# Optimization experiments

Measured on AMD Instinct MI355X. Metric: run time of the kernel, lower is better.

The kernel has to match this reference:

```python
import jax, jax.numpy as jnp
import numpy as np

D_MODEL = 1024
D_STATE = 32
EXPAND = 2
D_INNER = D_MODEL * EXPAND          # 2048
DT_RANK = D_MODEL // 16             # 64
LN_EPS = 1e-5


def setup_inputs() -> dict:
    key = jax.random.key(0)
    ks = jax.random.split(key, 9)
    s = 0.02
    x = jax.random.normal(ks[0], (2, 2048, D_MODEL), dtype=jnp.float32)
    W_in = jax.random.normal(ks[1], (2 * D_INNER, D_MODEL), dtype=jnp.float32) * s
    W_x = jax.random.normal(ks[2], (DT_RANK + 2 * D_STATE, D_INNER), dtype=jnp.float32) * s
    W_dt = jax.random.normal(ks[3], (D_INNER, DT_RANK), dtype=jnp.float32) * s
    b_dt = jax.random.normal(ks[4], (D_INNER,), dtype=jnp.float32) * s
    A_real0 = jax.random.normal(ks[5], (D_INNER, D_STATE), dtype=jnp.float32) * 0.5
    A_log_real = jnp.log(jnp.clip(-A_real0, 1e-4, None))
    A_imag = jax.random.normal(ks[6], (D_INNER, D_STATE), dtype=jnp.float32) * 0.1
    D_param = jnp.ones((D_INNER,), dtype=jnp.float32)
    W_out = jax.random.normal(ks[7], (D_MODEL, D_INNER), dtype=jnp.float32) * s
    ln_g = jnp.ones((D_MODEL,), dtype=jnp.float32)
    ln_b = jnp.zeros((D_MODEL,), dtype=jnp.float32)
    return {"x": x, "W_in": W_in, "W_x": W_x, "W_dt": W_dt, "b_dt": b_dt,
            "A_log_real": A_log_real, "A_imag": A_imag, "D_param": D_param,
            "W_out": W_out, "ln_g": ln_g, "ln_b": ln_b}


def _forward(x, W_in, W_x, W_dt, b_dt, A_log_real, A_imag, D_param, W_out, ln_g, ln_b):
    B, T, _ = x.shape
    residual = x
    # LayerNorm
    mu = jnp.mean(x, axis=-1, keepdims=True)
    var = jnp.mean((x - mu) ** 2, axis=-1, keepdims=True)
    xn = (x - mu) * jax.lax.rsqrt(var + LN_EPS) * ln_g + ln_b
    # in_proj -> (x_ssm, z)
    xz = jnp.einsum('btd,ed->bte', xn, W_in)            # (B,T,2*d_inner)
    x_ssm, z = jnp.split(xz, 2, axis=-1)
    # x_proj -> dt_low, B, C
    x_dbl = jnp.einsum('bte,re->btr', x_ssm, W_x)        # (B,T,dt_rank+2*d_state)
    dt_low = x_dbl[..., :DT_RANK]
    B_param = x_dbl[..., DT_RANK:DT_RANK + D_STATE]      # (B,T,N)
    C_param = x_dbl[..., DT_RANK + D_STATE:]             # (B,T,N)
    dt = jax.nn.softplus(jnp.einsum('btr,er->bte', dt_low, W_dt) + b_dt)  # (B,T,d_inner)
    # A = -exp(A_log_real) + i * A_imag, complex state split into (hr, hi)
    Ar = -jnp.exp(A_log_real)                             # (d_inner,N)
    Ai = A_imag

    def step(carry, inp):
        hr, hi = carry                                    # (B,d_inner,N)
        dt_t, B_t, C_t, x_t = inp                         # (B,d_inner),(B,N),(B,N),(B,d_inner)
        dtE = dt_t[:, :, None]                            # (B,d_inner,1)
        scale = jnp.exp(Ar[None] * dtE)
        ang = Ai[None] * dtE
        dAr = scale * jnp.cos(ang)
        dAi = scale * jnp.sin(ang)
        dBx = (dt_t * x_t)[:, :, None] * B_t[:, None, :]  # real input injection
        hr2 = dAr * hr - dAi * hi + dBx
        hi2 = dAr * hi + dAi * hr
        y = jnp.sum(hr2 * C_t[:, None, :], axis=-1)       # real part of (h * C).sum
        return (hr2, hi2), y

    h0 = jnp.zeros((B, D_INNER, D_STATE), dtype=x.dtype)
    xs = (jnp.transpose(dt, (1, 0, 2)), jnp.transpose(B_param, (1, 0, 2)),
          jnp.transpose(C_param, (1, 0, 2)), jnp.transpose(x_ssm, (1, 0, 2)))
    _, ys = jax.lax.scan(step, (h0, h0), xs)              # (T,B,d_inner)
    y = jnp.transpose(ys, (1, 0, 2)) + D_param * x_ssm
    y = y * jax.nn.silu(z)
    out = jnp.einsum('bte,de->btd', y, W_out)
    return residual + out  # dropout is identity at eval


def reference(x, W_in, W_x, W_dt, b_dt, A_log_real, A_imag, D_param, W_out, ln_g, ln_b):
    return _forward(x, W_in, W_x, W_dt, b_dt, A_log_real, A_imag, D_param, W_out, ln_g, ln_b)
```

## Files before the change

kernel.cpp:

```cpp
#include <hip/hip_runtime.h>
#include <math.h>

#define D_MODEL 1024
#define D_STATE 32
#define D_INNER 2048
#define DT_RANK 64
#define BT 4096
#define LN_EPS 1e-5f

typedef __attribute__((ext_vector_type(8))) short short8;
typedef __attribute__((ext_vector_type(4))) float f32x4;
typedef const __attribute__((address_space(1))) void* gp_t;
typedef __attribute__((address_space(3))) void* lp_t;

__device__ __forceinline__ ushort bf16r(float f) {
    unsigned u = __float_as_uint(f);
    u += 0x7fff + ((u >> 16) & 1);
    return (ushort)(u >> 16);
}

__global__ __launch_bounds__(256) void cvt_bf16(const float* __restrict__ in,
                                                ushort* __restrict__ out, int n4) {
    int i = blockIdx.x * 256 + threadIdx.x;
    if (i >= n4) return;
    float4 v = ((const float4*)in)[i];
    ushort4 o;
    o.x = bf16r(v.x); o.y = bf16r(v.y); o.z = bf16r(v.z); o.w = bf16r(v.w);
    ((ushort4*)out)[i] = o;
}

__global__ __launch_bounds__(256) void ln_kernel(const float* __restrict__ x,
                                                 const float* __restrict__ g,
                                                 const float* __restrict__ b,
                                                 ushort* __restrict__ xn) {
    int row = blockIdx.x;
    const float4* xr = (const float4*)(x + (size_t)row * D_MODEL);
    float4 v = xr[threadIdx.x];
    float s  = v.x + v.y + v.z + v.w;
    float ss = v.x*v.x + v.y*v.y + v.z*v.z + v.w*v.w;
    #pragma unroll
    for (int off = 32; off > 0; off >>= 1) {
        s  += __shfl_down(s,  off, 64);
        ss += __shfl_down(ss, off, 64);
    }
    __shared__ float rs[4], rss[4];
    int wave = threadIdx.x >> 6;
    if ((threadIdx.x & 63) == 0) { rs[wave] = s; rss[wave] = ss; }
    __syncthreads();
    s  = rs[0] + rs[1] + rs[2] + rs[3];
    ss = rss[0] + rss[1] + rss[2] + rss[3];
    float mu  = s * (1.f / D_MODEL);
    float var = ss * (1.f / D_MODEL) - mu * mu;
    float inv = rsqrtf(var + LN_EPS);
    float4 gv = ((const float4*)g)[threadIdx.x];
    float4 bv = ((const float4*)b)[threadIdx.x];
    ushort4 o;
    o.x = bf16r((v.x - mu) * inv * gv.x + bv.x);
    o.y = bf16r((v.y - mu) * inv * gv.y + bv.y);
    o.z = bf16r((v.z - mu) * inv * gv.z + bv.z);
    o.w = bf16r((v.w - mu) * inv * gv.w + bv.w);
    ((ushort4*)(xn + (size_t)row * D_MODEL))[threadIdx.x] = o;
}

template<int RESID>
__global__ __launch_bounds__(256) void gemm_bt_bf16(
    const ushort* __restrict__ A, const ushort* __restrict__ B,
    float* __restrict__ C, int ldc, int K,
    const float* __restrict__ resid)
{
    __shared__ __align__(16) ushort As[128 * 32];
    __shared__ __align__(16) ushort Bs[128 * 32];
    int tid = threadIdx.x;
    int bm = blockIdx.x * 128, bn = blockIdx.y * 128;
    int wave = tid >> 6, lane = tid & 63;
    int wm = (wave & 1) * 64, wn = (wave >> 1) * 64;
    int quad = lane >> 4, m16 = lane & 15;
    int grow = tid >> 2;
    int gcol = (tid & 3) * 8;
    const size_t a0 = (size_t)(bm + grow) * K + gcol;
    const size_t b0 = (size_t)(bn + grow) * K + gcol;
    char* asw = (char*)As + wave * 1024;
    char* bsw = (char*)Bs + wave * 1024;

    f32x4 acc[4][4] = {};
    for (int k0 = 0; k0 < K; k0 += 32) {
        __builtin_amdgcn_global_load_lds((gp_t)(A + a0 + k0),                 (lp_t)asw,          16, 0, 0);
        __builtin_amdgcn_global_load_lds((gp_t)(A + a0 + (size_t)64*K + k0),  (lp_t)(asw + 4096), 16, 0, 0);
        __builtin_amdgcn_global_load_lds((gp_t)(B + b0 + k0),                 (lp_t)bsw,          16, 0, 0);
        __builtin_amdgcn_global_load_lds((gp_t)(B + b0 + (size_t)64*K + k0),  (lp_t)(bsw + 4096), 16, 0, 0);
        __syncthreads();
        short8 af[4], bf[4];
        #pragma unroll
        for (int i = 0; i < 4; ++i)
            af[i] = *(const short8*)&As[(wm + i * 16 + m16) * 32 + quad * 8];
        #pragma unroll
        for (int j = 0; j < 4; ++j)
            bf[j] = *(const short8*)&Bs[(wn + j * 16 + m16) * 32 + quad * 8];
        #pragma unroll
        for (int i = 0; i < 4; ++i)
            #pragma unroll
            for (int j = 0; j < 4; ++j)
                acc[i][j] = __builtin_amdgcn_mfma_f32_16x16x32_bf16(
                    af[i], bf[j], acc[i][j], 0, 0, 0);
        __syncthreads();
    }
    #pragma unroll
    for (int i = 0; i < 4; ++i) {
        #pragma unroll
        for (int r = 0; r < 4; ++r) {
            int row = bm + wm + i * 16 + quad * 4 + r;
            #pragma unroll
            for (int j = 0; j < 4; ++j) {
                int col = bn + wn + j * 16 + m16;
                float v = acc[i][j][r];
                if (RESID) v += resid[(size_t)row * ldc + col];
                C[(size_t)row * ldc + col] = v;
            }
        }
    }
}

template<int ACT>
__global__ __launch_bounds__(256) void gemm_nt(const float* __restrict__ A, int lda,
                                               const float* __restrict__ B, int ldb,
                                               float* __restrict__ C, int ldc,
                                               int K,
                                               const float* __restrict__ bias) {
    __shared__ float As[16][68];
    __shared__ float Bs[16][68];
    int tid = threadIdx.x;
    int bm = blockIdx.x * 64;
    int bn = blockIdx.y * 64;
    int tx = tid & 15, ty = tid >> 4;
    int lr = tid >> 2;
    int lk = (tid & 3) << 2;
    const float* Ap = A + (size_t)(bm + lr) * lda + lk;
    const float* Bp = B + (size_t)(bn + lr) * ldb + lk;
    float acc[4][4] = {};
    for (int k0 = 0; k0 < K; k0 += 16) {
        float4 a4 = *(const float4*)(Ap + k0);
        float4 b4 = *(const float4*)(Bp + k0);
        As[lk+0][lr] = a4.x; As[lk+1][lr] = a4.y; As[lk+2][lr] = a4.z; As[lk+3][lr] = a4.w;
        Bs[lk+0][lr] = b4.x; Bs[lk+1][lr] = b4.y; Bs[lk+2][lr] = b4.z; Bs[lk+3][lr] = b4.w;
        __syncthreads();
        #pragma unroll
        for (int k = 0; k < 16; ++k) {
            float4 av = *(const float4*)&As[k][ty << 2];
            float4 bv = *(const float4*)&Bs[k][tx << 2];
            float ar[4] = {av.x, av.y, av.z, av.w};
            float br[4] = {bv.x, bv.y, bv.z, bv.w};
            #pragma unroll
            for (int i = 0; i < 4; ++i)
                #pragma unroll
                for (int j = 0; j < 4; ++j)
                    acc[i][j] = fmaf(ar[i], br[j], acc[i][j]);
        }
        __syncthreads();
    }
    #pragma unroll
    for (int i = 0; i < 4; ++i) {
        int row = bm + (ty << 2) + i;
        #pragma unroll
        for (int j = 0; j < 4; ++j) {
            int col = bn + (tx << 2) + j;
            float v = acc[i][j];
            if (bias)  v += bias[col];
            if (ACT == 1) v = (v > 20.f) ? v : __logf(1.f + __expf(v));
            C[(size_t)row * ldc + col] = v;
        }
    }
}

__global__ __launch_bounds__(256) void scan_kernel(
    const float* __restrict__ xz,
    const float* __restrict__ xdbl,
    const float* __restrict__ dtm,
    const float* __restrict__ A_log_real,
    const float* __restrict__ A_imag,
    const float* __restrict__ D_param,
    ushort* __restrict__ y)
{
    const int tid = threadIdx.x;
    const int s   = tid & 31;
    const int el  = tid >> 5;
    const int b   = blockIdx.x >> 8;
    const int e0  = (blockIdx.x & 255) << 3;
    const int e   = e0 + el;
    const int stt = tid >> 3;
    const int sk  = tid & 7;
    const int btt = tid >> 4;
    const int bk  = (tid & 15) << 2;

    __shared__ __align__(16) float dxz[2][8][32][4];
    __shared__ __align__(16) float bcs[2][32][64];
    __shared__ __align__(16) float red[8][32][36];

    const float Ar = -__expf(A_log_real[e * D_STATE + s]);
    const float Ai = A_imag[e * D_STATE + s];
    const float Dp = D_param[e];
    float hr = 0.f, hi = 0.f;
    const float* xzb = xz   + (size_t)b * 2048 * 4096;
    const float* xdb = xdbl + (size_t)b * 2048 * 128;
    const float* dtb = dtm  + (size_t)b * 2048 * 2048;
    ushort*      yb  = y    + (size_t)b * 2048 * 2048;

    float r_d, r_x, r_z;
    float4 r_bc0, r_bc1;
    {
        r_d = dtb[(size_t)stt * 2048 + e0 + sk];
        r_x = xzb[(size_t)stt * 4096 + e0 + sk];
        r_z = xzb[(size_t)stt * 4096 + 2048 + e0 + sk];
        r_bc0 = *(const float4*)&xdb[(size_t)btt * 128 + DT_RANK + bk];
        r_bc1 = *(const float4*)&xdb[(size_t)(btt + 16) * 128 + DT_RANK + bk];
        dxz[0][sk][stt][0] = r_d; dxz[0][sk][stt][1] = r_x; dxz[0][sk][stt][2] = r_z;
        *(float4*)&bcs[0][btt][bk]      = r_bc0;
        *(float4*)&bcs[0][btt + 16][bk] = r_bc1;
    }
    for (int c = 0; c < 64; ++c) {
        const int buf = c & 1;
        __syncthreads();
        if (c < 63) {
            const int tn = (c + 1) * 32;
            r_d = dtb[(size_t)(tn + stt) * 2048 + e0 + sk];
            r_x = xzb[(size_t)(tn + stt) * 4096 + e0 + sk];
            r_z = xzb[(size_t)(tn + stt) * 4096 + 2048 + e0 + sk];
            r_bc0 = *(const float4*)&xdb[(size_t)(tn + btt) * 128 + DT_RANK + bk];
            r_bc1 = *(const float4*)&xdb[(size_t)(tn + btt + 16) * 128 + DT_RANK + bk];
        }
        #pragma unroll 8
        for (int tt = 0; tt < 32; ++tt) {
            float4 dxv = *(const float4*)&dxz[buf][el][tt][0];
            float Bv = bcs[buf][tt][s];
            float Cv = bcs[buf][tt][32 + s];
            float dtv = dxv.x, xv = dxv.y;
            float sc  = __expf(Ar * dtv);
            float ang = Ai * dtv;
            float sa = __sinf(ang), ca = __cosf(ang);
            float dAr = sc * ca, dAi = sc * sa;
            float dBx = dtv * xv * Bv;
            float hr2 = dAr * hr - dAi * hi + dBx;
            hi = dAr * hi + dAi * hr;
            hr = hr2;
            red[el][tt][s] = hr * Cv;
        }
        float acc = 0.f;
        #pragma unroll
        for (int k = 0; k < 8; ++k) {
            float4 v = *(const float4*)&red[el][s][k * 4];
            acc += (v.x + v.y) + (v.z + v.w);
        }
        float xg = dxz[buf][el][s][1];
        float zg = dxz[buf][el][s][2];
        float sig = 1.f / (1.f + __expf(-zg));
        float yv  = (acc + Dp * xg) * zg * sig;
        yb[(size_t)(c * 32 + s) * 2048 + e] = bf16r(yv);
        if (c < 63) {
            const int nb = buf ^ 1;
            dxz[nb][sk][stt][0] = r_d; dxz[nb][sk][stt][1] = r_x; dxz[nb][sk][stt][2] = r_z;
            *(float4*)&bcs[nb][btt][bk]      = r_bc0;
            *(float4*)&bcs[nb][btt + 16][bk] = r_bc1;
        }
    }
}

extern "C" void kernel_launch(void* const* d_in, const int* in_sizes, int n_in,
                              void* d_out, int out_size, void* d_ws, size_t ws_size,
                              hipStream_t stream) {
    const float* x          = (const float*)d_in[0];
    const float* W_in       = (const float*)d_in[1];
    const float* W_x        = (const float*)d_in[2];
    const float* W_dt       = (const float*)d_in[3];
    const float* b_dt       = (const float*)d_in[4];
    const float* A_log_real = (const float*)d_in[5];
    const float* A_imag     = (const float*)d_in[6];
    const float* D_param    = (const float*)d_in[7];
    const float* W_out      = (const float*)d_in[8];
    const float* ln_g       = (const float*)d_in[9];
    const float* ln_b       = (const float*)d_in[10];
    float* out = (float*)d_out;

    char* ws = (char*)d_ws;
    float*  xz      = (float*) (ws);
    float*  dt      = (float*) (ws + ((size_t) 64 << 20));
    float*  xdbl    = (float*) (ws + ((size_t) 96 << 20));
    ushort* xn_bf   = (ushort*)(ws + ((size_t) 98 << 20));
    ushort* Win_bf  = (ushort*)(ws + ((size_t)106 << 20));
    ushort* y_bf    = (ushort*)(ws + ((size_t)106 << 20));
    ushort* Wout_bf = (ushort*)(ws + ((size_t)122 << 20));

    cvt_bf16<<<(4096*1024/4 + 255)/256, 256, 0, stream>>>(W_in,  Win_bf,  4096*1024/4);
    cvt_bf16<<<(1024*2048/4 + 255)/256, 256, 0, stream>>>(W_out, Wout_bf, 1024*2048/4);
    ln_kernel<<<BT, 256, 0, stream>>>(x, ln_g, ln_b, xn_bf);
    gemm_bt_bf16<0><<<dim3(BT/128, 4096/128), 256, 0, stream>>>(
        xn_bf, Win_bf, xz, 4096, D_MODEL, nullptr);
    gemm_nt<0><<<dim3(BT/64, 128/64), 256, 0, stream>>>(
        xz, 4096, W_x, D_INNER, xdbl, 128, D_INNER, nullptr);
    gemm_nt<1><<<dim3(BT/64, D_INNER/64), 256, 0, stream>>>(
        xdbl, 128, W_dt, DT_RANK, dt, D_INNER, DT_RANK, b_dt);
    scan_kernel<<<512, 256, 0, stream>>>(xz, xdbl, dt, A_log_real, A_imag,
                                         D_param, y_bf);
    gemm_bt_bf16<1><<<dim3(BT/128, D_MODEL/128), 256, 0, stream>>>(
        y_bf, Wout_bf, out, D_MODEL, D_INNER, x);
}
```

Measured before the change: 581.0 us.

## Fold x_proj into in_proj via precomputed W_x·W_in_x weight product

Precomputes the combined weight W_x times the x-half of W_in (via a transpose-convert and a small bf16 GEMM) and appends it as 128 extra rows to the bf16 in_proj weights. The in_proj GEMM then emits dt_low, B and C directly, which removes the separate fp32 x_proj GEMM over the 2048-wide x_ssm. The scan also switches to native sin/cos builtins on pre-scaled angles and XOR-swizzles its reduction buffer to avoid LDS bank conflicts. In exchange, rounding the combined weight and the activations to bf16 changes precision, and the weight-preprocessing kernels now run on every call.

```diff
diff --git a/kernel.cpp b/kernel.cpp
--- a/kernel.cpp
+++ b/kernel.cpp
@@ -6,6 +6,7 @@
 #define D_INNER 2048
 #define DT_RANK 64
 #define BT 4096
+#define XZLD 4224
 #define LN_EPS 1e-5f
 
 typedef __attribute__((ext_vector_type(8))) short short8;
@@ -27,6 +28,21 @@
     ushort4 o;
     o.x = bf16r(v.x); o.y = bf16r(v.y); o.z = bf16r(v.z); o.w = bf16r(v.w);
     ((ushort4*)out)[i] = o;
+}
+
+__global__ __launch_bounds__(256) void transpose_cvt(const float* __restrict__ in,
+                                                     ushort* __restrict__ out) {
+    __shared__ float tile[32][33];
+    int bx = blockIdx.x * 32;
+    int by = blockIdx.y * 32;
+    int tx = threadIdx.x & 31, ty = threadIdx.x >> 5;
+    #pragma unroll
+    for (int i = 0; i < 32; i += 8)
+        tile[ty + i][tx] = in[(size_t)(bx + ty + i) * 1024 + by + tx];
+    __syncthreads();
+    #pragma unroll
+    for (int i = 0; i < 32; i += 8)
+        out[(size_t)(by + ty + i) * 2048 + bx + tx] = bf16r(tile[tx][ty + i]);
 }
 
 __global__ __launch_bounds__(256) void ln_kernel(const float* __restrict__ x,
@@ -173,7 +189,6 @@
 
 __global__ __launch_bounds__(256) void scan_kernel(
     const float* __restrict__ xz,
-    const float* __restrict__ xdbl,
     const float* __restrict__ dtm,
     const float* __restrict__ A_log_real,
     const float* __restrict__ A_imag,
@@ -193,26 +208,27 @@
 
     __shared__ __align__(16) float dxz[2][8][32][4];
     __shared__ __align__(16) float bcs[2][32][64];
-    __shared__ __align__(16) float red[8][32][36];
-
-    const float Ar = -__expf(A_log_real[e * D_STATE + s]);
-    const float Ai = A_imag[e * D_STATE + s];
-    const float Dp = D_param[e];
+    __shared__ __align__(16) float red[8][32][32];
+
+    const float Ar   = -__expf(A_log_real[e * D_STATE + s]);
+    const float Ai2p = A_imag[e * D_STATE + s] * 0.15915494f;
+    const float Dp   = D_param[e];
     float hr = 0.f, hi = 0.f;
-    const float* xzb = xz   + (size_t)b * 2048 * 4096;
-    const float* xdb = xdbl + (size_t)b * 2048 * 128;
-    const float* dtb = dtm  + (size_t)b * 2048 * 2048;
-    ushort*      yb  = y    + (size_t)b * 2048 * 2048;
+    const float* xzb = xz + (size_t)b * 2048 * XZLD;
+    const float* bcb = xzb + 4096 + DT_RANK;
+    const float* dtb = dtm + (size_t)b * 2048 * 2048;
+    ushort*      yb  = y   + (size_t)b * 2048 * 2048;
+    const int sx4 = (s & 7) << 2;
 
     float r_d, r_x, r_z;
     float4 r_bc0, r_bc1;
     {
         r_d = dtb[(size_t)stt * 2048 + e0 + sk];
-        r_x = xzb[(size_t)stt * 4096 + e0 + sk];
-        r_z = xzb[(size_t)stt * 4096 + 2048 + e0 + sk];
-        r_bc0 = *(const float4*)&xdb[(size_t)btt * 128 + DT_RANK + bk];
-        r_bc1 = *(const float4*)&xdb[(size_t)(btt + 16) * 128 + DT_RANK + bk];
-        dxz[0][sk][stt][0] = r_d; dxz[0][sk][stt][1] = r_x; dxz[0][sk][stt][2] = r_z;
+        r_x = xzb[(size_t)stt * XZLD + e0 + sk];
+        r_z = xzb[(size_t)stt * XZLD + 2048 + e0 + sk];
+        r_bc0 = *(const float4*)&bcb[(size_t)btt * XZLD + bk];
+        r_bc1 = *(const float4*)&bcb[(size_t)(btt + 16) * XZLD + bk];
+        dxz[0][sk][stt][0] = r_d; dxz[0][sk][stt][2] = r_x; dxz[0][sk][stt][3] = r_z;
         *(float4*)&bcs[0][btt][bk]      = r_bc0;
         *(float4*)&bcs[0][btt + 16][bk] = r_bc1;
     }
@@ -222,41 +238,40 @@
         if (c < 63) {
             const int tn = (c + 1) * 32;
             r_d = dtb[(size_t)(tn + stt) * 2048 + e0 + sk];
-            r_x = xzb[(size_t)(tn + stt) * 4096 + e0 + sk];
-            r_z = xzb[(size_t)(tn + stt) * 4096 + 2048 + e0 + sk];
-            r_bc0 = *(const float4*)&xdb[(size_t)(tn + btt) * 128 + DT_RANK + bk];
-            r_bc1 = *(const float4*)&xdb[(size_t)(tn + btt + 16) * 128 + DT_RANK + bk];
+            r_x = xzb[(size_t)(tn + stt) * XZLD + e0 + sk];
+            r_z = xzb[(size_t)(tn + stt) * XZLD + 2048 + e0 + sk];
+            r_bc0 = *(const float4*)&bcb[(size_t)(tn + btt) * XZLD + bk];
+            r_bc1 = *(const float4*)&bcb[(size_t)(tn + btt + 16) * XZLD + bk];
         }
         #pragma unroll 8
         for (int tt = 0; tt < 32; ++tt) {
             float4 dxv = *(const float4*)&dxz[buf][el][tt][0];
             float Bv = bcs[buf][tt][s];
             float Cv = bcs[buf][tt][32 + s];
-            float dtv = dxv.x, xv = dxv.y;
-            float sc  = __expf(Ar * dtv);
-            float ang = Ai * dtv;
-            float sa = __sinf(ang), ca = __cosf(ang);
+            float dtv = dxv.x, xv = dxv.z;
+            float sc = __expf(Ar * dtv);
+            float u  = Ai2p * dtv;
+            float sa = __builtin_amdgcn_sinf(u);
+            float ca = __builtin_amdgcn_cosf(u);
             float dAr = sc * ca, dAi = sc * sa;
-            float dBx = dtv * xv * Bv;
+            float dBx = (dtv * xv) * Bv;
             float hr2 = dAr * hr - dAi * hi + dBx;
             hi = dAr * hi + dAi * hr;
             hr = hr2;
-            red[el][tt][s] = hr * Cv;
+            red[el][tt][s ^ ((tt & 7) << 2)] = hr * Cv;
         }
         float acc = 0.f;
         #pragma unroll
-        for (int k = 0; k < 8; ++k) {
-            float4 v = *(const float4*)&red[el][s][k * 4];
+        for (int p = 0; p < 8; ++p) {
+            float4 v = *(const float4*)&red[el][s][(p << 2) ^ sx4];
             acc += (v.x + v.y) + (v.z + v.w);
         }
-        float xg = dxz[buf][el][s][1];
-        float zg = dxz[buf][el][s][2];
-        float sig = 1.f / (1.f + __expf(-zg));
-        float yv  = (acc + Dp * xg) * zg * sig;
-        yb[(size_t)(c * 32 + s) * 2048 + e] = bf16r(yv);
+        float2 xzg = *(const float2*)&dxz[buf][el][s][2];
+        float sig = 1.f / (1.f + __expf(-xzg.y));
+        yb[(size_t)(c * 32 + s) * 2048 + e] = bf16r((acc + Dp * xzg.x) * xzg.y * sig);
         if (c < 63) {
             const int nb = buf ^ 1;
-            dxz[nb][sk][stt][0] = r_d; dxz[nb][sk][stt][1] = r_x; dxz[nb][sk][stt][2] = r_z;
+            dxz[nb][sk][stt][0] = r_d; dxz[nb][sk][stt][2] = r_x; dxz[nb][sk][stt][3] = r_z;
             *(float4*)&bcs[nb][btt][bk]      = r_bc0;
             *(float4*)&bcs[nb][btt + 16][bk] = r_bc1;
         }
@@ -281,24 +296,28 @@
 
     char* ws = (char*)d_ws;
     float*  xz      = (float*) (ws);
-    float*  dt      = (float*) (ws + ((size_t) 64 << 20));
-    float*  xdbl    = (float*) (ws + ((size_t) 96 << 20));
+    float*  dt      = (float*) (ws + ((size_t) 66 << 20));
     ushort* xn_bf   = (ushort*)(ws + ((size_t) 98 << 20));
-    ushort* Win_bf  = (ushort*)(ws + ((size_t)106 << 20));
-    ushort* y_bf    = (ushort*)(ws + ((size_t)106 << 20));
-    ushort* Wout_bf = (ushort*)(ws + ((size_t)122 << 20));
-
-    cvt_bf16<<<(4096*1024/4 + 255)/256, 256, 0, stream>>>(W_in,  Win_bf,  4096*1024/4);
-    cvt_bf16<<<(1024*2048/4 + 255)/256, 256, 0, stream>>>(W_out, Wout_bf, 1024*2048/4);
+    ushort* Waug    = (ushort*)(ws + ((size_t)106 << 20));
+    ushort* y_bf    = (ushort*)(ws + ((size_t)115 << 20));
+    ushort* Wout_bf = (ushort*)(ws + ((size_t)131 << 20));
+    float*  Wcomb   = (float*) (ws);
+    ushort* Wx_bf   = (ushort*)(ws + ((size_t)  1 << 20));
+    ushort* WinT_bf = (ushort*)(ws + ((size_t)  2 << 20));
+
+    cvt_bf16<<<4096, 256, 0, stream>>>(W_in,  Waug,    4096*1024/4);
+    cvt_bf16<<<2048, 256, 0, stream>>>(W_out, Wout_bf, 1024*2048/4);
+    cvt_bf16<<< 256, 256, 0, stream>>>(W_x,   Wx_bf,    128*2048/4);
+    transpose_cvt<<<dim3(64, 32), 256, 0, stream>>>(W_in, WinT_bf);
+    gemm_bt_bf16<0><<<dim3(1, 8), 256, 0, stream>>>(
+        Wx_bf, WinT_bf, Wcomb, 1024, 2048, nullptr);
+    cvt_bf16<<<128, 256, 0, stream>>>(Wcomb, Waug + (size_t)4096*1024, 128*1024/4);
     ln_kernel<<<BT, 256, 0, stream>>>(x, ln_g, ln_b, xn_bf);
-    gemm_bt_bf16<0><<<dim3(BT/128, 4096/128), 256, 0, stream>>>(
-        xn_bf, Win_bf, xz, 4096, D_MODEL, nullptr);
-    gemm_nt<0><<<dim3(BT/64, 128/64), 256, 0, stream>>>(
-        xz, 4096, W_x, D_INNER, xdbl, 128, D_INNER, nullptr);
+    gemm_bt_bf16<0><<<dim3(BT/128, XZLD/128), 256, 0, stream>>>(
+        xn_bf, Waug, xz, XZLD, D_MODEL, nullptr);
     gemm_nt<1><<<dim3(BT/64, D_INNER/64), 256, 0, stream>>>(
-        xdbl, 128, W_dt, DT_RANK, dt, D_INNER, DT_RANK, b_dt);
-    scan_kernel<<<512, 256, 0, stream>>>(xz, xdbl, dt, A_log_real, A_imag,
-                                         D_param, y_bf);
+        xz + 4096, XZLD, W_dt, DT_RANK, dt, D_INNER, DT_RANK, b_dt);
+    scan_kernel<<<512, 256, 0, stream>>>(xz, dt, A_log_real, A_imag, D_param, y_bf);
     gemm_bt_bf16<1><<<dim3(BT/128, D_MODEL/128), 256, 0, stream>>>(
         y_bf, Wout_bf, out, D_MODEL, D_INNER, x);
 }
```

Measured after the change: 509.7 us. -12.3%, faster.
